# Performance work log

Measured on AMD Instinct MI355X. Metric: run time of the kernel, lower is better.

## Reference

```python
import jax, jax.numpy as jnp
import numpy as np

V_CHUNK = 2048  # module default v_chunk


def _chunked_ce(h, W, labels, weights, v_chunk):
    """Weighted mean CE computed with a flash-style online logsumexp over
    vocab chunks, never materializing the full [N, V] logits tensor."""
    N, D = h.shape
    V = W.shape[0]
    n_chunks = V // v_chunk
    Wc = W.reshape(n_chunks, v_chunk, D)          # [C, vc, D]
    offs = jnp.arange(n_chunks) * v_chunk          # chunk start indices
    rows = jnp.arange(N)

    def body(carry, xs):
        m, s, lab = carry                          # running max, sum(exp), label logit
        Wk, off = xs
        logits = h @ Wk.T                          # [N, vc] chunk logits
        cmax = logits.max(axis=1)
        m_new = jnp.maximum(m, cmax)
        s = s * jnp.exp(m - m_new) + jnp.exp(logits - m_new[:, None]).sum(axis=1)
        idx = labels - off
        in_chunk = (idx >= 0) & (idx < v_chunk)
        gathered = logits[rows, jnp.clip(idx, 0, v_chunk - 1)]
        lab = lab + jnp.where(in_chunk, gathered, jnp.float32(0))
        return (m_new, s, lab), None

    init = (jnp.full((N,), -jnp.inf, dtype=h.dtype),
            jnp.zeros((N,), dtype=h.dtype),
            jnp.zeros((N,), dtype=h.dtype))
    # checkpoint the body so chunk logits are recomputed, not stored
    (m, s, lab), _ = jax.lax.scan(jax.checkpoint(body), init, (Wc, offs))
    lse = m + jnp.log(s)                           # [N]
    nll = lse - lab                                # [N] per-token NLL
    return jnp.sum(weights * nll) / jnp.sum(weights)


def setup_inputs() -> dict:
    key = jax.random.key(0)
    k1, k2, k3, k4 = jax.random.split(key, 4)
    B, S, D, V = 1, 4096, 2048, 65536
    h = jax.random.normal(k1, (B, S, D), dtype=jnp.float32)
    W = jax.random.normal(k2, (V, D), dtype=jnp.float32) * 0.02
    labels = jax.random.randint(k3, (B, S), 0, V, dtype=jnp.int64)
    loss_weights = jax.random.uniform(k4, (B, S), dtype=jnp.float32)
    return {"hidden_states": h, "labels": labels,
            "loss_weights": loss_weights, "W": W}


def reference(hidden_states, labels, loss_weights, W):
    D = hidden_states.shape[-1]
    h_flat = hidden_states.reshape(-1, D)
    labels_flat = labels.reshape(-1)
    weights_flat = loss_weights.reshape(-1)
    return _chunked_ce(h_flat, W, labels_flat, weights_flat, V_CHUNK)
```

## Files before the change

### kernel.cpp

```cpp
#include <hip/hip_runtime.h>


typedef __attribute__((ext_vector_type(4)))  float f32x4;
typedef __attribute__((ext_vector_type(8)))  float f32x8;
typedef __attribute__((ext_vector_type(4)))  int   i32x4;

#define N_TOK 4096
#define DIM   2048
#define VOCAB 65536
#define BM    256
#define BN    256
#define BK    128
#define NT    (DIM / BK)
#define NCH   (VOCAB / BN)
#define NTB   (N_TOK / BM)

__device__ __forceinline__ void gload_lds16(const void* g, void* l) {
    __builtin_amdgcn_global_load_lds(
        (const __attribute__((address_space(1))) void*)g,
        (__attribute__((address_space(3))) void*)l, 16, 0, 0);
}

__device__ __forceinline__ void bar() {
    asm volatile("" ::: "memory");
    __builtin_amdgcn_s_barrier();
    asm volatile("" ::: "memory");
}

__global__ __launch_bounds__(256) void convert_f32_i8(
    const float* __restrict__ src, signed char* __restrict__ dst,
    long n, float scale)
{
    long i = ((long)blockIdx.x * 256 + threadIdx.x) * 8;
    if (i + 8 > n) return;
    f32x8 v = *(const f32x8*)(src + i);
    signed char o[8];
    #pragma unroll
    for (int j = 0; j < 8; ++j) {
        float x = v[j] * scale;
        x = fminf(fmaxf(x, -127.0f), 127.0f);
        o[j] = (signed char)__float2int_rn(x);
    }
    *(uint2*)(dst + i) = *(const uint2*)o;
}

__global__ __launch_bounds__(512, 2) void gemm_lse(
    const signed char* __restrict__ h8,
    const signed char* __restrict__ W8,
    float* __restrict__ part_m, float* __restrict__ part_s, int chunk0)
{
    __shared__ unsigned char A_lds[2][32768];
    __shared__ unsigned char B_lds[2][32768];

    const int tid  = threadIdx.x;
    const int lane = tid & 63;
    const int w    = tid >> 6;
    const int wm   = w >> 2;
    const int wn   = w & 3;

    const int nwg  = gridDim.x;
    const int orig = blockIdx.x;
    const int q8 = nwg >> 3, r8 = nwg & 7;
    const int xcd = orig & 7;
    const int wg  = (xcd < r8 ? xcd * (q8 + 1) : r8 * (q8 + 1) + (xcd - r8) * q8)
                    + (orig >> 3);
    const int tok_blk = wg & (NTB - 1);
    const int voc_blk = wg >> 4;

    const long arow0 = (long)tok_blk * BM;
    const signed char* Ab = h8 + arow0 * DIM;
    const signed char* Bb = W8 + (long)voc_blk * BN * DIM;

    i32x4 acc[8][4];
    #pragma unroll
    for (int i = 0; i < 8; ++i)
        #pragma unroll
        for (int j = 0; j < 4; ++j)
            acc[i][j] = (i32x4){0, 0, 0, 0};

    const long soff = (long)(tid >> 3) * DIM + ((tid & 7) ^ ((tid >> 3) & 7)) * 16;
    const int  sdb  = w * 1024;

#define SW_A(t, j, PD)                                                        \
    gload_lds16(Ab + (t) * BK + soff + (long)(j) * 64 * DIM,                  \
                (char*)&A_lds[PD][0] + sdb + (j) * 8192);
#define SW_B(t, j, PD)                                                        \
    gload_lds16(Bb + (t) * BK + soff + (long)(j) * 64 * DIM,                  \
                (char*)&B_lds[PD][0] + sdb + (j) * 8192);

    const int lrow = lane & 15;
    const int cxe0 = (((lane >> 4) + 0) ^ (lane & 7)) * 16;
    const int cxe1 = (((lane >> 4) + 4) ^ (lane & 7)) * 16;

#define LDF2(D, BASE, ROWB)                                                   \
    D[0] = *(const i32x4*)((BASE) + (ROWB) + cxe0);                           \
    D[1] = *(const i32x4*)((BASE) + (ROWB) + cxe1);

#define MFMA32(MB, AR)                                                        \
    __builtin_amdgcn_s_setprio(1);                                            \
    _Pragma("unroll")                                                         \
    for (int g = 0; g < 2; ++g)                                               \
        _Pragma("unroll")                                                     \
        for (int m = 0; m < 4; ++m)                                           \
            _Pragma("unroll")                                                 \
            for (int nf = 0; nf < 4; ++nf)                                    \
                acc[(MB) + m][nf] = __builtin_amdgcn_mfma_i32_16x16x64_i8(    \
                    AR[m][g], bR[nf][g], acc[(MB) + m][nf], 0, 0, 0);         \
    __builtin_amdgcn_s_setprio(0);

#define WAITL()                                                               \
    asm volatile("s_waitcnt lgkmcnt(0)" ::: "memory");                        \
    __builtin_amdgcn_sched_barrier(0);

#define KTILE(P, t)                                                           \
    {                                                                         \
        const char* Ah = (const char*)&A_lds[P][0] + wm * 16384;              \
        const char* Bh = (const char*)&B_lds[P][0] + wn * 8192;               \
        i32x4 bR[4][2], aR[4][2];                                             \
                    \
        LDF2(bR[0], Bh, 0 * 2048 + lrow * 128)                                \
        LDF2(bR[1], Bh, 1 * 2048 + lrow * 128)                                \
        LDF2(bR[2], Bh, 2 * 2048 + lrow * 128)                                \
        LDF2(bR[3], Bh, 3 * 2048 + lrow * 128)                                \
        LDF2(aR[0], Ah, 0 * 2048 + lrow * 128)                                \
        LDF2(aR[1], Ah, 1 * 2048 + lrow * 128)                                \
        LDF2(aR[2], Ah, 2 * 2048 + lrow * 128)                                \
        LDF2(aR[3], Ah, 3 * 2048 + lrow * 128)                                \
        if ((t) + 1 < NT) {                                                   \
            SW_A((t) + 1, 0, (P) ^ 1) SW_A((t) + 1, 1, (P) ^ 1)               \
            SW_A((t) + 1, 2, (P) ^ 1) SW_A((t) + 1, 3, (P) ^ 1)               \
        }                                                                     \
        bar(); WAITL()                                                        \
        MFMA32(0, aR)                                                         \
               \
        LDF2(aR[0], Ah, 4 * 2048 + lrow * 128)                                \
        LDF2(aR[1], Ah, 5 * 2048 + lrow * 128)                                \
        LDF2(aR[2], Ah, 6 * 2048 + lrow * 128)                                \
        LDF2(aR[3], Ah, 7 * 2048 + lrow * 128)                                \
        bar();                                                                \
        if ((t) + 2 < NT) {                                                   \
            SW_B((t) + 2, 0, P) SW_B((t) + 2, 1, P)                           \
            SW_B((t) + 2, 2, P) SW_B((t) + 2, 3, P)                           \
        }                                                                     \
        WAITL()                                                               \
        MFMA32(4, aR)                                                         \
        if ((t) < NT - 2) { asm volatile("s_waitcnt vmcnt(4)" ::: "memory"); }\
        else              { asm volatile("s_waitcnt vmcnt(0)" ::: "memory"); }\
        bar();                                                                \
    }

    SW_A(0, 0, 0) SW_A(0, 1, 0) SW_A(0, 2, 0) SW_A(0, 3, 0)
    SW_B(0, 0, 0) SW_B(0, 1, 0) SW_B(0, 2, 0) SW_B(0, 3, 0)
    SW_B(1, 0, 1) SW_B(1, 1, 1) SW_B(1, 2, 1) SW_B(1, 3, 1)
    asm volatile("s_waitcnt vmcnt(4)" ::: "memory");
    bar();

    for (int t = 0; t < NT; t += 2) {
        KTILE(0, t)
        KTILE(1, t + 1)
    }
#undef KTILE
#undef SW_A
#undef SW_B
#undef LDF2
#undef MFMA32
#undef WAITL

    const float INV = 1.0f / 16384.0f;
    float* red_m = (float*)&A_lds[0][0];
    float* red_s = ((float*)&A_lds[0][0]) + 1024;
    #pragma unroll
    for (int mf = 0; mf < 8; ++mf) {
        #pragma unroll
        for (int r = 0; r < 4; ++r) {
            float v0 = (float)acc[mf][0][r] * INV;
            float v1 = (float)acc[mf][1][r] * INV;
            float v2 = (float)acc[mf][2][r] * INV;
            float v3 = (float)acc[mf][3][r] * INV;
            float mx = fmaxf(fmaxf(v0, v1), fmaxf(v2, v3));
            #pragma unroll
            for (int msk = 1; msk < 16; msk <<= 1)
                mx = fmaxf(mx, __shfl_xor(mx, msk, 64));
            float se = __expf(v0 - mx) + __expf(v1 - mx) +
                       __expf(v2 - mx) + __expf(v3 - mx);
            #pragma unroll
            for (int msk = 1; msk < 16; msk <<= 1)
                se += __shfl_xor(se, msk, 64);
            if ((lane & 15) == 0) {
                const int row = wm * 128 + mf * 16 + (lane >> 4) * 4 + r;
                red_m[row * 4 + wn] = mx;
                red_s[row * 4 + wn] = se;
            }
        }
    }
    __syncthreads();
    if (tid < 256) {
        float M = red_m[tid * 4], S = red_s[tid * 4];
        #pragma unroll
        for (int j = 1; j < 4; ++j) {
            const float m2 = red_m[tid * 4 + j], s2 = red_s[tid * 4 + j];
            const float Mn = fmaxf(M, m2);
            S = S * __expf(M - Mn) + s2 * __expf(m2 - Mn);
            M = Mn;
        }
        part_m[(arow0 + tid) * NCH + chunk0 + voc_blk] = M;
        part_s[(arow0 + tid) * NCH + chunk0 + voc_blk] = S;
    }
}

__global__ __launch_bounds__(256) void label_dot(
    const float* __restrict__ h, const float* __restrict__ W,
    const void* __restrict__ labels, float* __restrict__ lab_logit)
{
    bool is64 = true;
    #pragma unroll
    for (int i = 0; i < 8; ++i) {
        long long v = ((const long long*)labels)[i];
        if (v < 0 || v >= VOCAB) is64 = false;
    }
    const int t = blockIdx.x;
    const int lab = is64 ? (int)((const long long*)labels)[t]
                         : ((const int*)labels)[t];
    const float4* hp = (const float4*)(h + (long)t * DIM);
    const float4* wp = (const float4*)(W + (long)lab * DIM);
    float s = 0.f;
    #pragma unroll
    for (int j = 0; j < 2; ++j) {
        const float4 a = hp[threadIdx.x + j * 256];
        const float4 b = wp[threadIdx.x + j * 256];
        s += a.x * b.x + a.y * b.y + a.z * b.z + a.w * b.w;
    }
    #pragma unroll
    for (int msk = 1; msk < 64; msk <<= 1) s += __shfl_xor(s, msk, 64);
    __shared__ float ps[4];
    if ((threadIdx.x & 63) == 0) ps[threadIdx.x >> 6] = s;
    __syncthreads();
    if (threadIdx.x == 0) lab_logit[t] = ps[0] + ps[1] + ps[2] + ps[3];
}

__global__ __launch_bounds__(256) void finalize_nll(
    const float* __restrict__ part_m, const float* __restrict__ part_s,
    const float* __restrict__ lab_logit, const float* __restrict__ wts,
    float* __restrict__ wnll)
{
    const int t    = blockIdx.x * 4 + (threadIdx.x >> 6);
    const int lane = threadIdx.x & 63;
    float m = -3.4e38f, s = 0.f;
    #pragma unroll
    for (int j = 0; j < 4; ++j) {
        const int c = j * 64 + lane;
        const float pm = part_m[(long)t * NCH + c];
        const float ps = part_s[(long)t * NCH + c];
        const float M = fmaxf(m, pm);
        s = s * __expf(m - M) + ps * __expf(pm - M);
        m = M;
    }
    #pragma unroll
    for (int msk = 1; msk < 64; msk <<= 1) {
        const float om = __shfl_xor(m, msk, 64);
        const float os = __shfl_xor(s, msk, 64);
        const float M = fmaxf(m, om);
        s = s * __expf(m - M) + os * __expf(om - M);
        m = M;
    }
    if (lane == 0) {
        const float lse = m + logf(s);
        wnll[t] = wts[t] * (lse - lab_logit[t]);
    }
}

__global__ __launch_bounds__(1024) void final_reduce(
    const float* __restrict__ wnll, const float* __restrict__ wts,
    float* __restrict__ out)
{
    float a = 0.f, b = 0.f;
    #pragma unroll
    for (int j = 0; j < 4; ++j) {
        const int i = threadIdx.x + j * 1024;
        a += wnll[i];
        b += wts[i];
    }
    #pragma unroll
    for (int msk = 1; msk < 64; msk <<= 1) {
        a += __shfl_xor(a, msk, 64);
        b += __shfl_xor(b, msk, 64);
    }
    __shared__ float pa[16], pb[16];
    if ((threadIdx.x & 63) == 0) {
        pa[threadIdx.x >> 6] = a;
        pb[threadIdx.x >> 6] = b;
    }
    __syncthreads();
    if (threadIdx.x == 0) {
        float A = 0.f, B = 0.f;
        #pragma unroll
        for (int i = 0; i < 16; ++i) { A += pa[i]; B += pb[i]; }
        out[0] = A / B;
    }
}

extern "C" void kernel_launch(void* const* d_in, const int* in_sizes, int n_in,
                              void* d_out, int out_size, void* d_ws, size_t ws_size,
                              hipStream_t stream)
{
    const float* h      = (const float*)d_in[0];
    const void*  labels = d_in[1];
    const float* wts    = (const float*)d_in[2];
    const float* W      = (const float*)d_in[3];
    float* out = (float*)d_out;

    char* ws = (char*)d_ws;
    signed char*    h8        = (signed char*)(ws);
    float*          part_m    = (float*)(ws + (16u << 20));
    float*          part_s    = (float*)(ws + (24u << 20));
    float*          lab_logit = (float*)(ws + (32u << 20));
    float*          wnll      = (float*)(ws + (32u << 20) + 16384);
    signed char*    wseg      = (signed char*)(ws + (32u << 20) + 32768);
    const size_t base = (size_t)(32u << 20) + 32768;

    long segmax = 0;
    if (ws_size > base) segmax = (long)((ws_size - base) / (size_t)DIM);
    segmax &= ~255L;
    if (segmax > VOCAB) segmax = VOCAB;
    if (segmax < 256)   segmax = 256;

    convert_f32_i8<<<(N_TOK * DIM) / (256 * 8), 256, 0, stream>>>(
        h, h8, (long)N_TOK * DIM, 16.0f);

    for (long v0 = 0; v0 < VOCAB; v0 += segmax) {
        const long rows = (VOCAB - v0) < segmax ? (VOCAB - v0) : segmax;
        convert_f32_i8<<<(int)(rows * DIM / (256 * 8)), 256, 0, stream>>>(
            W + v0 * DIM, wseg, rows * (long)DIM, 1024.0f);
        const int nwg = (int)(rows / BM) * NTB;
        gemm_lse<<<nwg, 512, 0, stream>>>(h8, wseg, part_m, part_s,
                                          (int)(v0 / BN));
    }

    label_dot<<<N_TOK, 256, 0, stream>>>(h, W, labels, lab_logit);

    finalize_nll<<<N_TOK / 4, 256, 0, stream>>>(part_m, part_s, lab_logit,
                                                wts, wnll);

    final_reduce<<<1, 1024, 0, stream>>>(wnll, wts, out);
}
```

Before: 765.4 us.

## Shrink GEMM tile to 128x256x64 with simpler double-buffered pipeline for higher occupancy

Cuts the token tile from 256 to 128 rows and the K step from 128 to 64, which shrinks LDS use and accumulator registers so four workgroups can be resident per CU instead of two. The LDS layout drops the XOR swizzle and the two-stage B prefetch is replaced by a plain one-ahead double buffer that waits for all loads to finish each K step. The aim is more latency hiding through occupancy, at the cost of lower data reuse per tile, twice as many K iterations and barriers, and possible LDS bank conflicts now that the swizzle is gone. The launch grid now uses BN to count vocab blocks so that it stays consistent with the new tiling.

```diff
diff --git a/kernel.cpp b/kernel.cpp
--- a/kernel.cpp
+++ b/kernel.cpp
@@ -8,9 +8,9 @@
 #define N_TOK 4096
 #define DIM   2048
 #define VOCAB 65536
-#define BM    256
+#define BM    128
 #define BN    256
-#define BK    128
+#define BK    64
 #define NT    (DIM / BK)
 #define NCH   (VOCAB / BN)
 #define NTB   (N_TOK / BM)
@@ -44,19 +44,19 @@
     *(uint2*)(dst + i) = *(const uint2*)o;
 }
 
-__global__ __launch_bounds__(512, 2) void gemm_lse(
+__global__ __launch_bounds__(512, 4) void gemm_lse(
     const signed char* __restrict__ h8,
     const signed char* __restrict__ W8,
     float* __restrict__ part_m, float* __restrict__ part_s, int chunk0)
 {
-    __shared__ unsigned char A_lds[2][32768];
-    __shared__ unsigned char B_lds[2][32768];
+    __shared__ unsigned char A_lds[2][8192];
+    __shared__ unsigned char B_lds[2][16384];
 
     const int tid  = threadIdx.x;
     const int lane = tid & 63;
     const int w    = tid >> 6;
-    const int wm   = w >> 2;
-    const int wn   = w & 3;
+    const int wmr  = w >> 2;
+    const int wnc  = w & 3;
 
     const int nwg  = gridDim.x;
     const int orig = blockIdx.x;
@@ -65,118 +65,79 @@
     const int wg  = (xcd < r8 ? xcd * (q8 + 1) : r8 * (q8 + 1) + (xcd - r8) * q8)
                     + (orig >> 3);
     const int tok_blk = wg & (NTB - 1);
-    const int voc_blk = wg >> 4;
+    const int voc_blk = wg >> 5;
 
     const long arow0 = (long)tok_blk * BM;
     const signed char* Ab = h8 + arow0 * DIM;
     const signed char* Bb = W8 + (long)voc_blk * BN * DIM;
 
-    i32x4 acc[8][4];
-    #pragma unroll
-    for (int i = 0; i < 8; ++i)
+    i32x4 acc[4][4];
+    #pragma unroll
+    for (int i = 0; i < 4; ++i)
         #pragma unroll
         for (int j = 0; j < 4; ++j)
             acc[i][j] = (i32x4){0, 0, 0, 0};
 
-    const long soff = (long)(tid >> 3) * DIM + ((tid & 7) ^ ((tid >> 3) & 7)) * 16;
+    const long soff = (long)(tid >> 2) * DIM + (tid & 3) * 16;
     const int  sdb  = w * 1024;
 
-#define SW_A(t, j, PD)                                                        \
-    gload_lds16(Ab + (t) * BK + soff + (long)(j) * 64 * DIM,                  \
-                (char*)&A_lds[PD][0] + sdb + (j) * 8192);
-#define SW_B(t, j, PD)                                                        \
-    gload_lds16(Bb + (t) * BK + soff + (long)(j) * 64 * DIM,                  \
+#define SW_A(t, PD)                                                           \
+    gload_lds16(Ab + (t) * BK + soff, (char*)&A_lds[PD][0] + sdb);
+#define SW_B(t, PD, j)                                                        \
+    gload_lds16(Bb + (t) * BK + soff + (long)(j) * 128 * DIM,                 \
                 (char*)&B_lds[PD][0] + sdb + (j) * 8192);
 
-    const int lrow = lane & 15;
-    const int cxe0 = (((lane >> 4) + 0) ^ (lane & 7)) * 16;
-    const int cxe1 = (((lane >> 4) + 4) ^ (lane & 7)) * 16;
-
-#define LDF2(D, BASE, ROWB)                                                   \
-    D[0] = *(const i32x4*)((BASE) + (ROWB) + cxe0);                           \
-    D[1] = *(const i32x4*)((BASE) + (ROWB) + cxe1);
-
-#define MFMA32(MB, AR)                                                        \
-    __builtin_amdgcn_s_setprio(1);                                            \
-    _Pragma("unroll")                                                         \
-    for (int g = 0; g < 2; ++g)                                               \
+    const int rbase = (lane & 15) * 64 + (lane >> 4) * 16;
+
+#define KTILE(CUR, NXT, t)                                                    \
+    {                                                                         \
+        if ((t) + 1 < NT) {                                                   \
+            SW_A((t) + 1, NXT)                                                \
+            SW_B((t) + 1, NXT, 0)                                             \
+            SW_B((t) + 1, NXT, 1)                                             \
+        }                                                                     \
+        const char* Ah = (const char*)&A_lds[CUR][0] + wmr * 4096 + rbase;    \
+        const char* Bh = (const char*)&B_lds[CUR][0] + wnc * 4096 + rbase;    \
+        i32x4 aR[4], bR[4];                                                   \
+        _Pragma("unroll")                                                     \
+        for (int m = 0; m < 4; ++m) aR[m] = *(const i32x4*)(Ah + m * 1024);   \
+        _Pragma("unroll")                                                     \
+        for (int n = 0; n < 4; ++n) bR[n] = *(const i32x4*)(Bh + n * 1024);   \
+        __builtin_amdgcn_s_setprio(1);                                        \
         _Pragma("unroll")                                                     \
         for (int m = 0; m < 4; ++m)                                           \
             _Pragma("unroll")                                                 \
-            for (int nf = 0; nf < 4; ++nf)                                    \
-                acc[(MB) + m][nf] = __builtin_amdgcn_mfma_i32_16x16x64_i8(    \
-                    AR[m][g], bR[nf][g], acc[(MB) + m][nf], 0, 0, 0);         \
-    __builtin_amdgcn_s_setprio(0);
-
-#define WAITL()                                                               \
-    asm volatile("s_waitcnt lgkmcnt(0)" ::: "memory");                        \
-    __builtin_amdgcn_sched_barrier(0);
-
-#define KTILE(P, t)                                                           \
-    {                                                                         \
-        const char* Ah = (const char*)&A_lds[P][0] + wm * 16384;              \
-        const char* Bh = (const char*)&B_lds[P][0] + wn * 8192;               \
-        i32x4 bR[4][2], aR[4][2];                                             \
-                    \
-        LDF2(bR[0], Bh, 0 * 2048 + lrow * 128)                                \
-        LDF2(bR[1], Bh, 1 * 2048 + lrow * 128)                                \
-        LDF2(bR[2], Bh, 2 * 2048 + lrow * 128)                                \
-        LDF2(bR[3], Bh, 3 * 2048 + lrow * 128)                                \
-        LDF2(aR[0], Ah, 0 * 2048 + lrow * 128)                                \
-        LDF2(aR[1], Ah, 1 * 2048 + lrow * 128)                                \
-        LDF2(aR[2], Ah, 2 * 2048 + lrow * 128)                                \
-        LDF2(aR[3], Ah, 3 * 2048 + lrow * 128)                                \
-        if ((t) + 1 < NT) {                                                   \
-            SW_A((t) + 1, 0, (P) ^ 1) SW_A((t) + 1, 1, (P) ^ 1)               \
-            SW_A((t) + 1, 2, (P) ^ 1) SW_A((t) + 1, 3, (P) ^ 1)               \
-        }                                                                     \
-        bar(); WAITL()                                                        \
-        MFMA32(0, aR)                                                         \
-               \
-        LDF2(aR[0], Ah, 4 * 2048 + lrow * 128)                                \
-        LDF2(aR[1], Ah, 5 * 2048 + lrow * 128)                                \
-        LDF2(aR[2], Ah, 6 * 2048 + lrow * 128)                                \
-        LDF2(aR[3], Ah, 7 * 2048 + lrow * 128)                                \
+            for (int n = 0; n < 4; ++n)                                       \
+                acc[m][n] = __builtin_amdgcn_mfma_i32_16x16x64_i8(            \
+                    aR[m], bR[n], acc[m][n], 0, 0, 0);                        \
+        __builtin_amdgcn_s_setprio(0);                                        \
+        asm volatile("s_waitcnt vmcnt(0)" ::: "memory");                      \
         bar();                                                                \
-        if ((t) + 2 < NT) {                                                   \
-            SW_B((t) + 2, 0, P) SW_B((t) + 2, 1, P)                           \
-            SW_B((t) + 2, 2, P) SW_B((t) + 2, 3, P)                           \
-        }                                                                     \
-        WAITL()                                                               \
-        MFMA32(4, aR)                                                         \
-        if ((t) < NT - 2) { asm volatile("s_waitcnt vmcnt(4)" ::: "memory"); }\
-        else              { asm volatile("s_waitcnt vmcnt(0)" ::: "memory"); }\
-        bar();                                                                \
-    }
-
-    SW_A(0, 0, 0) SW_A(0, 1, 0) SW_A(0, 2, 0) SW_A(0, 3, 0)
-    SW_B(0, 0, 0) SW_B(0, 1, 0) SW_B(0, 2, 0) SW_B(0, 3, 0)
-    SW_B(1, 0, 1) SW_B(1, 1, 1) SW_B(1, 2, 1) SW_B(1, 3, 1)
-    asm volatile("s_waitcnt vmcnt(4)" ::: "memory");
+    }
+
+    SW_A(0, 0) SW_B(0, 0, 0) SW_B(0, 0, 1)
+    asm volatile("s_waitcnt vmcnt(0)" ::: "memory");
     bar();
 
     for (int t = 0; t < NT; t += 2) {
-        KTILE(0, t)
-        KTILE(1, t + 1)
+        KTILE(0, 1, t)
+        KTILE(1, 0, t + 1)
     }
 #undef KTILE
 #undef SW_A
 #undef SW_B
-#undef LDF2
-#undef MFMA32
-#undef WAITL
 
     const float INV = 1.0f / 16384.0f;
     float* red_m = (float*)&A_lds[0][0];
-    float* red_s = ((float*)&A_lds[0][0]) + 1024;
-    #pragma unroll
-    for (int mf = 0; mf < 8; ++mf) {
+    float* red_s = ((float*)&A_lds[0][0]) + 512;
+    #pragma unroll
+    for (int m = 0; m < 4; ++m) {
         #pragma unroll
         for (int r = 0; r < 4; ++r) {
-            float v0 = (float)acc[mf][0][r] * INV;
-            float v1 = (float)acc[mf][1][r] * INV;
-            float v2 = (float)acc[mf][2][r] * INV;
-            float v3 = (float)acc[mf][3][r] * INV;
+            float v0 = (float)acc[m][0][r] * INV;
+            float v1 = (float)acc[m][1][r] * INV;
+            float v2 = (float)acc[m][2][r] * INV;
+            float v3 = (float)acc[m][3][r] * INV;
             float mx = fmaxf(fmaxf(v0, v1), fmaxf(v2, v3));
             #pragma unroll
             for (int msk = 1; msk < 16; msk <<= 1)
@@ -187,14 +148,14 @@
             for (int msk = 1; msk < 16; msk <<= 1)
                 se += __shfl_xor(se, msk, 64);
             if ((lane & 15) == 0) {
-                const int row = wm * 128 + mf * 16 + (lane >> 4) * 4 + r;
-                red_m[row * 4 + wn] = mx;
-                red_s[row * 4 + wn] = se;
+                const int row = wmr * 64 + m * 16 + (lane >> 4) * 4 + r;
+                red_m[row * 4 + wnc] = mx;
+                red_s[row * 4 + wnc] = se;
             }
         }
     }
     __syncthreads();
-    if (tid < 256) {
+    if (tid < BM) {
         float M = red_m[tid * 4], S = red_s[tid * 4];
         #pragma unroll
         for (int j = 1; j < 4; ++j) {
@@ -331,7 +292,7 @@
         const long rows = (VOCAB - v0) < segmax ? (VOCAB - v0) : segmax;
         convert_f32_i8<<<(int)(rows * DIM / (256 * 8)), 256, 0, stream>>>(
             W + v0 * DIM, wseg, rows * (long)DIM, 1024.0f);
-        const int nwg = (int)(rows / BM) * NTB;
+        const int nwg = (int)(rows / BN) * NTB;
         gemm_lse<<<nwg, 512, 0, stream>>>(h8, wseg, part_m, part_s,
                                           (int)(v0 / BN));
     }
```

Result: slower. 796.0 us (+4.0%).
